# Optimization experiments

Hardware: AMD Instinct MI355X
Metric: run time of the kernel (lower is better)

## Reference

```python
import jax, jax.numpy as jnp
import numpy as np

H = 64   # hidden size
V = 29   # vocab / feature size
SOS = 27 # start-token index set to 1 in the initial one-hot


def _cell(x, h, c, Wih, Whh, bih, bhh):
    # PyTorch LSTMCell gate order: i, f, g, o
    g = x @ Wih.T + h @ Whh.T + bih + bhh
    i, f, gg, o = jnp.split(g, 4, axis=-1)
    c = jax.nn.sigmoid(f) * c + jax.nn.sigmoid(i) * jnp.tanh(gg)
    h = jax.nn.sigmoid(o) * jnp.tanh(c)
    return h, c


def setup_inputs() -> dict:
    key = jax.random.key(0)
    ks = iter(jax.random.split(key, 32))
    T, B = 1024, 512
    def p(shape, scale=0.05):
        return jax.random.normal(next(ks), shape, dtype=jnp.float32) * scale
    inp = {"input_seq": jax.random.normal(next(ks), (T, B, V), dtype=jnp.float32)}
    inp.update(
        enc_Wih0=p((4 * H, V)), enc_Whh0=p((4 * H, H)), enc_bih0=p((4 * H,)), enc_bhh0=p((4 * H,)),
        enc_Wih1=p((4 * H, H)), enc_Whh1=p((4 * H, H)), enc_bih1=p((4 * H,)), enc_bhh1=p((4 * H,)),
        d1_Wih=p((4 * H, V)), d1_Whh=p((4 * H, H)), d1_bih=p((4 * H,)), d1_bhh=p((4 * H,)),
        d2_Wih=p((4 * H, H)), d2_Whh=p((4 * H, H)), d2_bih=p((4 * H,)), d2_bhh=p((4 * H,)),
        cls_W=p((V, H)), cls_b=p((V,)),
    )
    return inp


def reference(input_seq, enc_Wih0, enc_Whh0, enc_bih0, enc_bhh0,
              enc_Wih1, enc_Whh1, enc_bih1, enc_bhh1,
              d1_Wih, d1_Whh, d1_bih, d1_bhh,
              d2_Wih, d2_Whh, d2_bih, d2_bhh,
              cls_W, cls_b):
    T, B, _ = input_seq.shape
    dt = input_seq.dtype
    z = jnp.zeros((B, H), dt)

    def layer(x_seq, Wih, Whh, bih, bhh):
        def step(carry, x):
            h, c = _cell(x, carry[0], carry[1], Wih, Whh, bih, bhh)
            return (h, c), h
        (h, c), ys = jax.lax.scan(step, (z, z), x_seq)
        return ys, h, c

    # 2-layer encoder LSTM with zero initial state
    y1, _, _ = layer(input_seq, enc_Wih0, enc_Whh0, enc_bih0, enc_bhh0)
    _, h1, c1 = layer(y1, enc_Wih1, enc_Whh1, enc_bih1, enc_bhh1)  # top-layer final (h, c)

    let0 = jnp.zeros((B, V), dt).at[:, SOS].set(1.0)

    def dec_step(carry, _):
        h1, c1, h2, c2, let = carry
        h1, c1 = _cell(let, h1, c1, d1_Wih, d1_Whh, d1_bih, d1_bhh)
        h2, c2 = _cell(h1, h2, c2, d2_Wih, d2_Whh, d2_bih, d2_bhh)
        pred = h2 @ cls_W.T + cls_b  # [B, V]
        idx = jnp.argmax(pred, axis=-1)  # [B]
        # Faithful to original bug: sets column idx[b] to 1 for ALL rows, for each b
        let = jnp.zeros((B, V), pred.dtype).at[:, idx].set(1.0)
        return (h1, c1, h2, c2, let), pred

    _, outputs = jax.lax.scan(dec_step, (h1, c1, z, z, let0), None, length=T)
    return outputs  # [T, B, V]
```

## Files before the change

### kernel.cpp

```cpp
#include <hip/hip_runtime.h>
#include <math.h>

#define TSTEPS 1024
#define BATCH  512
#define HID    64
#define VOC    29
#define SOS    27
#define MASK29 0x1FFFFFFFu

#define ENC_BLOCKS 256
#define DEC_BLOCKS 256
#define NTHREADS   512

__device__ __forceinline__ float frcp(float x){ return __builtin_amdgcn_rcpf(x); }
__device__ __forceinline__ float sigmf(float x){ return frcp(1.0f + __expf(-x)); }
__device__ __forceinline__ float tanhfast(float x){ return 1.0f - 2.0f*frcp(1.0f + __expf(2.0f*x)); }

__global__ __attribute__((amdgpu_flat_work_group_size(NTHREADS,NTHREADS), amdgpu_waves_per_eu(2,2)))
void enc_kernel(const float* __restrict__ x,
                const float* __restrict__ Wih0, const float* __restrict__ Whh0,
                const float* __restrict__ bih0, const float* __restrict__ bhh0,
                const float* __restrict__ Wih1, const float* __restrict__ Whh1,
                const float* __restrict__ bih1, const float* __restrict__ bhh1,
                float* __restrict__ h1g, float* __restrict__ c1g)
{
  const int tid = threadIdx.x;
  const int b0  = blockIdx.x * 2;
  const bool g0 = tid < 256;
  const int  r  = g0 ? tid : (tid-256);

  __shared__ __align__(16) float xs[2][32];
  __shared__ __align__(16) float h0s[2][HID], h1s[2][HID];
  __shared__ __align__(16) float gA[2][256], gB[2][256];

  float wh[64], w2[64];
  if (g0){
    #pragma unroll
    for (int k=0;k<64;k++) wh[k] = Whh0[r*64+k];
    #pragma unroll
    for (int k=0;k<29;k++) w2[k] = Wih0[r*29+k];
    #pragma unroll
    for (int k=29;k<64;k++) w2[k] = 0.f;
  } else {
    #pragma unroll
    for (int k=0;k<64;k++){ wh[k] = Whh1[r*64+k]; w2[k] = Wih1[r*64+k]; }
  }
  const float bias = g0 ? (bih0[r]+bhh0[r]) : (bih1[r]+bhh1[r]);

  float creg = 0.f;
  if (tid < 128){ int u=tid>>6,k=tid&63; h0s[u][k]=0.f; h1s[u][k]=0.f; }

  const int pidx = tid - 448;
  const bool pf  = (pidx >= 0) && (pidx < 2*VOC);
  const int prow = pf ? (pidx/VOC) : 0;
  const int pcol = pf ? (pidx%VOC) : 0;
  if (pf) xs[prow][pcol] = x[(size_t)(b0+prow)*VOC + pcol];
  __syncthreads();

  for (int t=0;t<=TSTEPS;t++){
    float xv = 0.f;
    if (pf && t+1 < TSTEPS)
      xv = x[(size_t)(t+1)*BATCH*VOC + (size_t)(b0+prow)*VOC + pcol];

    if (g0){
      if (t < TSTEPS){
        #pragma unroll
        for (int u=0;u<2;u++){
          float a0=bias,a1=0.f,a2=0.f,a3=0.f;
          const float4* xv4 = (const float4*)xs[u];
          #pragma unroll
          for (int c=0;c<7;c++){
            float4 q=xv4[c];
            a0=fmaf(q.x,w2[4*c+0],a0); a1=fmaf(q.y,w2[4*c+1],a1);
            a2=fmaf(q.z,w2[4*c+2],a2); a3=fmaf(q.w,w2[4*c+3],a3);
          }
          a0=fmaf(xs[u][28],w2[28],a0);
          const float4* h4=(const float4*)h0s[u];
          #pragma unroll
          for (int c=0;c<16;c++){
            float4 q=h4[c];
            a0=fmaf(q.x,wh[4*c+0],a0); a1=fmaf(q.y,wh[4*c+1],a1);
            a2=fmaf(q.z,wh[4*c+2],a2); a3=fmaf(q.w,wh[4*c+3],a3);
          }
          gA[u][r]=(a0+a1)+(a2+a3);
        }
      }
    } else {
      if (t >= 1){
        #pragma unroll
        for (int u=0;u<2;u++){
          float a0=bias,a1=0.f,a2=0.f,a3=0.f;
          const float4* i4=(const float4*)h0s[u];
          const float4* h4=(const float4*)h1s[u];
          #pragma unroll
          for (int c=0;c<16;c++){
            float4 q=i4[c], w=h4[c];
            a0=fmaf(q.x,w2[4*c+0],a0); a1=fmaf(q.y,w2[4*c+1],a1);
            a2=fmaf(q.z,w2[4*c+2],a2); a3=fmaf(q.w,w2[4*c+3],a3);
            a0=fmaf(w.x,wh[4*c+0],a0); a1=fmaf(w.y,wh[4*c+1],a1);
            a2=fmaf(w.z,wh[4*c+2],a2); a3=fmaf(w.w,wh[4*c+3],a3);
          }
          gB[u][r]=(a0+a1)+(a2+a3);
        }
      }
    }
    __syncthreads();
    if (tid < 128){
      if (t < TSTEPS){
        int u=tid>>6,k=tid&63;
        float ig=gA[u][k],fg=gA[u][64+k],gg=gA[u][128+k],og=gA[u][192+k];
        float c=sigmf(fg)*creg + sigmf(ig)*tanhfast(gg);
        creg=c; h0s[u][k]=sigmf(og)*tanhfast(c);
      }
    } else if (tid < 384){
      if (t >= 1){
        int tt=tid-256,u=tt>>6,k=tt&63;
        float ig=gB[u][k],fg=gB[u][64+k],gg=gB[u][128+k],og=gB[u][192+k];
        float c=sigmf(fg)*creg + sigmf(ig)*tanhfast(gg);
        creg=c; h1s[u][k]=sigmf(og)*tanhfast(c);
      }
    }
    if (pf && t+1 < TSTEPS) xs[prow][pcol] = xv;
    __syncthreads();
  }

  if (tid >= 256 && tid < 384){
    int tt=tid-256,u=tt>>6,k=tt&63;
    h1g[(b0+u)*HID+k]=h1s[u][k];
    c1g[(b0+u)*HID+k]=creg;
  }
}

__global__ __attribute__((amdgpu_flat_work_group_size(NTHREADS,NTHREADS), amdgpu_waves_per_eu(2,2)))
void dec_kernel(const float* __restrict__ h1gp, const float* __restrict__ c1gp,
                const float* __restrict__ W1ih, const float* __restrict__ W1hh,
                const float* __restrict__ b1ih, const float* __restrict__ b1hh,
                const float* __restrict__ W2ih, const float* __restrict__ W2hh,
                const float* __restrict__ b2ih, const float* __restrict__ b2hh,
                const float* __restrict__ clsW, const float* __restrict__ clsb,
                float* __restrict__ out,
                unsigned long long* __restrict__ lvl1)
{
  const int tid  = threadIdx.x;
  const int r    = tid >> 1;
  const int p    = tid & 1;
  const int b0   = blockIdx.x * 2;
  const unsigned grp = blockIdx.x & 15;
  const unsigned idx = blockIdx.x >> 4;

  __shared__ __align__(16) float clsW_s[VOC][68];
  __shared__ __align__(16) float clsb_s[32];
  __shared__ __align__(16) float gl[2][256];
  __shared__ __align__(16) float h1s[2][HID], h2s[2][HID];
  __shared__ unsigned maskLDS;

  for (int i=tid;i<VOC*HID;i+=NTHREADS) clsW_s[i/HID][i%HID] = clsW[i];
  if (tid<VOC) clsb_s[tid]=clsb[tid];

  float w1h[32], w2i[32], w2h[32], wi1c[15];
  #pragma unroll
  for (int k=0;k<32;k++){
    w1h[k]=W1hh[r*HID+32*p+k];
    w2i[k]=W2ih[r*HID+32*p+k];
    w2h[k]=W2hh[r*HID+32*p+k];
  }
  const int cbase = p ? 15 : 0;
  const int cn    = p ? 14 : 15;
  #pragma unroll
  for (int j=0;j<15;j++) wi1c[j] = (j<cn) ? W1ih[r*VOC+cbase+j] : 0.f;
  const float biasg = p ? 0.f : (b1ih[r]+b1hh[r]);
  const float bias2 = p ? 0.f : (b2ih[r]+b2hh[r]);

  float c1reg=0.f, c2reg=0.f;
  if (tid<128){
    int u=tid>>6,k=tid&63;
    h1s[u][k]=h1gp[(b0+u)*HID+k];
    c1reg    =c1gp[(b0+u)*HID+k];
    h2s[u][k]=0.f;
  }
  __syncthreads();

  float hd1[2];
  #pragma unroll
  for (int u=0;u<2;u++){
    float a0=0.f,a1=0.f,a2=0.f,a3=0.f;
    const float4* h4=(const float4*)(h1s[u]+32*p);
    #pragma unroll
    for (int c=0;c<8;c++){
      float4 q=h4[c];
      a0=fmaf(q.x,w1h[4*c+0],a0); a1=fmaf(q.y,w1h[4*c+1],a1);
      a2=fmaf(q.z,w1h[4*c+2],a2); a3=fmaf(q.w,w1h[4*c+3],a3);
    }
    hd1[u]=(a0+a1)+(a2+a3);
  }

  unsigned mask = 1u<<SOS;

  for (int s=0;s<TSTEPS;s++){
    #pragma unroll
    for (int u=0;u<2;u++){
      float it = biasg;
      #pragma unroll
      for (int j=0;j<15;j++)
        it += ((mask>>(cbase+j))&1u) ? wi1c[j] : 0.f;
      float v = it + hd1[u];
      v += __shfl_xor(v,1);
      if (!p) gl[u][r] = v;
    }
    __syncthreads();
    if (tid<128){
      int u=tid>>6,k=tid&63;
      float ig=gl[u][k],fg=gl[u][64+k],gg=gl[u][128+k],og=gl[u][192+k];
      float c=sigmf(fg)*c1reg+sigmf(ig)*tanhfast(gg);
      c1reg=c; h1s[u][k]=sigmf(og)*tanhfast(c);
    }
    __syncthreads();
    #pragma unroll
    for (int u=0;u<2;u++){
      float a0=bias2,a1=0.f,a2=0.f,a3=0.f;
      const float4* i4=(const float4*)(h1s[u]+32*p);
      const float4* h4=(const float4*)(h2s[u]+32*p);
      #pragma unroll
      for (int c=0;c<8;c++){
        float4 q=i4[c], w=h4[c];
        a0=fmaf(q.x,w2i[4*c+0],a0); a1=fmaf(q.y,w2i[4*c+1],a1);
        a2=fmaf(q.z,w2i[4*c+2],a2); a3=fmaf(q.w,w2i[4*c+3],a3);
        a0=fmaf(w.x,w2h[4*c+0],a0); a1=fmaf(w.y,w2h[4*c+1],a1);
        a2=fmaf(w.z,w2h[4*c+2],a2); a3=fmaf(w.w,w2h[4*c+3],a3);
      }
      float v=(a0+a1)+(a2+a3);
      v += __shfl_xor(v,1);
      if (!p) gl[u][r]=v;
    }
    __syncthreads();
    if (tid<128){
      int u=tid>>6,k=tid&63;
      float ig=gl[u][k],fg=gl[u][64+k],gg=gl[u][128+k],og=gl[u][192+k];
      float c=sigmf(fg)*c2reg+sigmf(ig)*tanhfast(gg);
      c2reg=c; h2s[u][k]=sigmf(og)*tanhfast(c);
    }
    __syncthreads();
    if (tid<64){
      int row=tid>>5, v=tid&31;
      float pv = -INFINITY;
      if (v<VOC){
        float a0=clsb_s[v],a1=0.f,a2=0.f,a3=0.f;
        const float4* h4=(const float4*)h2s[row];
        #pragma unroll
        for (int c=0;c<16;c++){
          float4 q=h4[c];
          a0=fmaf(q.x,clsW_s[v][4*c+0],a0); a1=fmaf(q.y,clsW_s[v][4*c+1],a1);
          a2=fmaf(q.z,clsW_s[v][4*c+2],a2); a3=fmaf(q.w,clsW_s[v][4*c+3],a3);
        }
        pv=(a0+a1)+(a2+a3);
        out[((size_t)s*BATCH + (size_t)(b0+row))*VOC + v]=pv;
      }
      int ix=v;
      #pragma unroll
      for (int off=16; off>0; off>>=1){
        float ov=__shfl_xor(pv,off);
        int   oi=__shfl_xor(ix,off);
        if (ov>pv || (ov==pv && oi<ix)){ pv=ov; ix=oi; }
      }
      unsigned bit = 1u<<ix;
      unsigned mb  = bit | __shfl_xor(bit,32);
      if (tid==0 && s+1<TSTEPS)
        __hip_atomic_fetch_or(&lvl1[(size_t)grp*TSTEPS+s],
                              (unsigned long long)mb | (1ULL<<(32+idx)),
                              __ATOMIC_RELAXED, __HIP_MEMORY_SCOPE_AGENT);
    }
    if (s+1<TSTEPS){
      #pragma unroll
      for (int u=0;u<2;u++){
        float a0=0.f,a1=0.f,a2=0.f,a3=0.f;
        const float4* h4=(const float4*)(h1s[u]+32*p);
        #pragma unroll
        for (int c=0;c<8;c++){
          float4 q=h4[c];
          a0=fmaf(q.x,w1h[4*c+0],a0); a1=fmaf(q.y,w1h[4*c+1],a1);
          a2=fmaf(q.z,w1h[4*c+2],a2); a3=fmaf(q.w,w1h[4*c+3],a3);
        }
        hd1[u]=(a0+a1)+(a2+a3);
      }
      if (tid<64){
        while (true){
          unsigned long long u64 = 0;
          if (tid<16)
            u64 = __hip_atomic_load(&lvl1[(size_t)tid*TSTEPS+s],
                                    __ATOMIC_RELAXED, __HIP_MEMORY_SCOPE_AGENT);
          bool ok = (tid>=16) || ((unsigned)(u64>>32) == 0xFFFFu);
          if (__ballot(ok) == ~0ull){
            unsigned m = (tid<16) ? ((unsigned)u64 & MASK29) : 0u;
            m |= __shfl_xor(m,1); m |= __shfl_xor(m,2);
            m |= __shfl_xor(m,4); m |= __shfl_xor(m,8);
            if (tid==0) maskLDS = m;
            break;
          }
        }
      }
      __syncthreads();
      mask = maskLDS;
    }
  }
}

extern "C" void kernel_launch(void* const* d_in, const int* in_sizes, int n_in,
                              void* d_out, int out_size, void* d_ws, size_t ws_size,
                              hipStream_t stream)
{
  const float* x     = (const float*)d_in[0];
  const float* eWih0 = (const float*)d_in[1];
  const float* eWhh0 = (const float*)d_in[2];
  const float* ebih0 = (const float*)d_in[3];
  const float* ebhh0 = (const float*)d_in[4];
  const float* eWih1 = (const float*)d_in[5];
  const float* eWhh1 = (const float*)d_in[6];
  const float* ebih1 = (const float*)d_in[7];
  const float* ebhh1 = (const float*)d_in[8];
  const float* d1Wih = (const float*)d_in[9];
  const float* d1Whh = (const float*)d_in[10];
  const float* d1bih = (const float*)d_in[11];
  const float* d1bhh = (const float*)d_in[12];
  const float* d2Wih = (const float*)d_in[13];
  const float* d2Whh = (const float*)d_in[14];
  const float* d2bih = (const float*)d_in[15];
  const float* d2bhh = (const float*)d_in[16];
  const float* clsW  = (const float*)d_in[17];
  const float* clsb  = (const float*)d_in[18];
  float* out = (float*)d_out;

  float* h1g = (float*)d_ws;
  float* c1g = h1g + BATCH*HID;
  unsigned long long* lvl1 = (unsigned long long*)((char*)d_ws + (size_t)(2*BATCH*HID)*sizeof(float));

  hipMemsetAsync(lvl1, 0, 16*TSTEPS*sizeof(unsigned long long), stream);

  enc_kernel<<<ENC_BLOCKS, NTHREADS, 0, stream>>>(
      x, eWih0,eWhh0,ebih0,ebhh0, eWih1,eWhh1,ebih1,ebhh1, h1g,c1g);

  void* args[] = { (void*)&h1g, (void*)&c1g,
                   (void*)&d1Wih,(void*)&d1Whh,(void*)&d1bih,(void*)&d1bhh,
                   (void*)&d2Wih,(void*)&d2Whh,(void*)&d2bih,(void*)&d2bhh,
                   (void*)&clsW,(void*)&clsb,(void*)&out,(void*)&lvl1 };
  hipLaunchCooperativeKernel((void*)dec_kernel, dim3(DEC_BLOCKS), dim3(NTHREADS),
                             args, 0, stream);
}
```

Measured before the change: 5.881 ms.

## Restructure encoder to one batch row per block and fuse decoder gate activations

The encoder now gives each block a single batch row: two threads per gate row split the dot product, and layer 0 and layer 1 run one after the other within a timestep. It launches 512 blocks with waves_per_eu raised to 4. The decoder now assigns four threads per hidden unit, each holding all four gates. After a shuffle reduction every thread applies the activations itself, which removes the separate gate-to-LDS exchange and two barriers per step. The input-weight table moves to LDS and h2 is double-buffered. The encoder now has a longer serial chain per step (two sequential layers with four barriers), and the decoder uses more registers and LDS.

```diff
diff --git a/kernel.cpp b/kernel.cpp
--- a/kernel.cpp
+++ b/kernel.cpp
@@ -8,7 +8,7 @@
 #define SOS    27
 #define MASK29 0x1FFFFFFFu
 
-#define ENC_BLOCKS 256
+#define ENC_BLOCKS 512
 #define DEC_BLOCKS 256
 #define NTHREADS   512
 
@@ -16,7 +16,7 @@
 __device__ __forceinline__ float sigmf(float x){ return frcp(1.0f + __expf(-x)); }
 __device__ __forceinline__ float tanhfast(float x){ return 1.0f - 2.0f*frcp(1.0f + __expf(2.0f*x)); }
 
-__global__ __attribute__((amdgpu_flat_work_group_size(NTHREADS,NTHREADS), amdgpu_waves_per_eu(2,2)))
+__global__ __attribute__((amdgpu_flat_work_group_size(NTHREADS,NTHREADS), amdgpu_waves_per_eu(4,4)))
 void enc_kernel(const float* __restrict__ x,
                 const float* __restrict__ Wih0, const float* __restrict__ Whh0,
                 const float* __restrict__ bih0, const float* __restrict__ bhh0,
@@ -25,109 +25,99 @@
                 float* __restrict__ h1g, float* __restrict__ c1g)
 {
   const int tid = threadIdx.x;
-  const int b0  = blockIdx.x * 2;
-  const bool g0 = tid < 256;
-  const int  r  = g0 ? tid : (tid-256);
-
-  __shared__ __align__(16) float xs[2][32];
-  __shared__ __align__(16) float h0s[2][HID], h1s[2][HID];
-  __shared__ __align__(16) float gA[2][256], gB[2][256];
-
-  float wh[64], w2[64];
-  if (g0){
-    #pragma unroll
-    for (int k=0;k<64;k++) wh[k] = Whh0[r*64+k];
-    #pragma unroll
-    for (int k=0;k<29;k++) w2[k] = Wih0[r*29+k];
-    #pragma unroll
-    for (int k=29;k<64;k++) w2[k] = 0.f;
-  } else {
-    #pragma unroll
-    for (int k=0;k<64;k++){ wh[k] = Whh1[r*64+k]; w2[k] = Wih1[r*64+k]; }
-  }
-  const float bias = g0 ? (bih0[r]+bhh0[r]) : (bih1[r]+bhh1[r]);
+  const int r   = tid >> 1;
+  const int p   = tid & 1;
+  const int b0  = blockIdx.x;
+
+  __shared__ __align__(16) float xs[32];
+  __shared__ __align__(16) float g0[256];
+  __shared__ __align__(16) float h0s[HID], h1s[HID];
+
+  float w0h[32], w1i[32], w1h[32], w0i[15];
+  #pragma unroll
+  for (int k=0;k<32;k++){
+    w0h[k]=Whh0[r*HID+32*p+k];
+    w1i[k]=Wih1[r*HID+32*p+k];
+    w1h[k]=Whh1[r*HID+32*p+k];
+  }
+  const int cb = p*15, cn = p?14:15;
+  #pragma unroll
+  for (int j=0;j<15;j++) w0i[j] = (j<cn)? Wih0[r*VOC+cb+j] : 0.f;
+  const float bias0 = p?0.f:(bih0[r]+bhh0[r]);
+  const float bias1 = p?0.f:(bih1[r]+bhh1[r]);
 
   float creg = 0.f;
-  if (tid < 128){ int u=tid>>6,k=tid&63; h0s[u][k]=0.f; h1s[u][k]=0.f; }
-
-  const int pidx = tid - 448;
-  const bool pf  = (pidx >= 0) && (pidx < 2*VOC);
-  const int prow = pf ? (pidx/VOC) : 0;
-  const int pcol = pf ? (pidx%VOC) : 0;
-  if (pf) xs[prow][pcol] = x[(size_t)(b0+prow)*VOC + pcol];
+  if (tid<64) h0s[tid]=0.f;
+  if (tid>=64 && tid<128) h1s[tid-64]=0.f;
+  if (tid>=186 && tid<189) xs[29+(tid-186)]=0.f;
+
+  const int pfc = tid-128;
+  const bool ispf = (pfc>=0) && (pfc<VOC);
+  if (ispf) xs[pfc] = x[(size_t)b0*VOC + pfc];
   __syncthreads();
 
-  for (int t=0;t<=TSTEPS;t++){
-    float xv = 0.f;
-    if (pf && t+1 < TSTEPS)
-      xv = x[(size_t)(t+1)*BATCH*VOC + (size_t)(b0+prow)*VOC + pcol];
-
-    if (g0){
-      if (t < TSTEPS){
-        #pragma unroll
-        for (int u=0;u<2;u++){
-          float a0=bias,a1=0.f,a2=0.f,a3=0.f;
-          const float4* xv4 = (const float4*)xs[u];
-          #pragma unroll
-          for (int c=0;c<7;c++){
-            float4 q=xv4[c];
-            a0=fmaf(q.x,w2[4*c+0],a0); a1=fmaf(q.y,w2[4*c+1],a1);
-            a2=fmaf(q.z,w2[4*c+2],a2); a3=fmaf(q.w,w2[4*c+3],a3);
-          }
-          a0=fmaf(xs[u][28],w2[28],a0);
-          const float4* h4=(const float4*)h0s[u];
-          #pragma unroll
-          for (int c=0;c<16;c++){
-            float4 q=h4[c];
-            a0=fmaf(q.x,wh[4*c+0],a0); a1=fmaf(q.y,wh[4*c+1],a1);
-            a2=fmaf(q.z,wh[4*c+2],a2); a3=fmaf(q.w,wh[4*c+3],a3);
-          }
-          gA[u][r]=(a0+a1)+(a2+a3);
-        }
-      }
-    } else {
-      if (t >= 1){
-        #pragma unroll
-        for (int u=0;u<2;u++){
-          float a0=bias,a1=0.f,a2=0.f,a3=0.f;
-          const float4* i4=(const float4*)h0s[u];
-          const float4* h4=(const float4*)h1s[u];
-          #pragma unroll
-          for (int c=0;c<16;c++){
-            float4 q=i4[c], w=h4[c];
-            a0=fmaf(q.x,w2[4*c+0],a0); a1=fmaf(q.y,w2[4*c+1],a1);
-            a2=fmaf(q.z,w2[4*c+2],a2); a3=fmaf(q.w,w2[4*c+3],a3);
-            a0=fmaf(w.x,wh[4*c+0],a0); a1=fmaf(w.y,wh[4*c+1],a1);
-            a2=fmaf(w.z,wh[4*c+2],a2); a3=fmaf(w.w,wh[4*c+3],a3);
-          }
-          gB[u][r]=(a0+a1)+(a2+a3);
-        }
-      }
-    }
-    __syncthreads();
-    if (tid < 128){
-      if (t < TSTEPS){
-        int u=tid>>6,k=tid&63;
-        float ig=gA[u][k],fg=gA[u][64+k],gg=gA[u][128+k],og=gA[u][192+k];
-        float c=sigmf(fg)*creg + sigmf(ig)*tanhfast(gg);
-        creg=c; h0s[u][k]=sigmf(og)*tanhfast(c);
-      }
-    } else if (tid < 384){
-      if (t >= 1){
-        int tt=tid-256,u=tt>>6,k=tt&63;
-        float ig=gB[u][k],fg=gB[u][64+k],gg=gB[u][128+k],og=gB[u][192+k];
-        float c=sigmf(fg)*creg + sigmf(ig)*tanhfast(gg);
-        creg=c; h1s[u][k]=sigmf(og)*tanhfast(c);
-      }
-    }
-    if (pf && t+1 < TSTEPS) xs[prow][pcol] = xv;
-    __syncthreads();
-  }
-
-  if (tid >= 256 && tid < 384){
-    int tt=tid-256,u=tt>>6,k=tt&63;
-    h1g[(b0+u)*HID+k]=h1s[u][k];
-    c1g[(b0+u)*HID+k]=creg;
+  for (int t=0;t<TSTEPS;t++){
+    float xn=0.f;
+    if (ispf && t+1<TSTEPS)
+      xn = x[(size_t)(t+1)*BATCH*VOC + (size_t)b0*VOC + pfc];
+
+    {
+      float a0=bias0,a1=0.f,a2=0.f,a3=0.f;
+      #pragma unroll
+      for (int j=0;j<15;j++){
+        float acc = fmaf(xs[cb+j], w0i[j], (j&3)==0?a0:((j&3)==1?a1:((j&3)==2?a2:a3)));
+        if ((j&3)==0) a0=acc; else if ((j&3)==1) a1=acc; else if ((j&3)==2) a2=acc; else a3=acc;
+      }
+      const float4* hv=(const float4*)(h0s+32*p);
+      #pragma unroll
+      for (int c=0;c<8;c++){
+        float4 q=hv[c];
+        a0=fmaf(q.x,w0h[4*c+0],a0); a1=fmaf(q.y,w0h[4*c+1],a1);
+        a2=fmaf(q.z,w0h[4*c+2],a2); a3=fmaf(q.w,w0h[4*c+3],a3);
+      }
+      float v=(a0+a1)+(a2+a3);
+      v += __shfl_xor(v,1);
+      if (!p) g0[r]=v;
+    }
+    __syncthreads();
+    if (tid<64){
+      int k=tid;
+      float ig=g0[k],fg=g0[64+k],gg=g0[128+k],og=g0[192+k];
+      float c=sigmf(fg)*creg+sigmf(ig)*tanhfast(gg);
+      creg=c; h0s[k]=sigmf(og)*tanhfast(c);
+    }
+    __syncthreads();
+    {
+      float a0=bias1,a1=0.f,a2=0.f,a3=0.f;
+      const float4* iv=(const float4*)(h0s+32*p);
+      const float4* hv=(const float4*)(h1s+32*p);
+      #pragma unroll
+      for (int c=0;c<8;c++){
+        float4 q=iv[c], w=hv[c];
+        a0=fmaf(q.x,w1i[4*c+0],a0); a1=fmaf(q.y,w1i[4*c+1],a1);
+        a2=fmaf(q.z,w1i[4*c+2],a2); a3=fmaf(q.w,w1i[4*c+3],a3);
+        a0=fmaf(w.x,w1h[4*c+0],a0); a1=fmaf(w.y,w1h[4*c+1],a1);
+        a2=fmaf(w.z,w1h[4*c+2],a2); a3=fmaf(w.w,w1h[4*c+3],a3);
+      }
+      float v=(a0+a1)+(a2+a3);
+      v += __shfl_xor(v,1);
+      if (!p) g0[r]=v;
+    }
+    __syncthreads();
+    if (tid>=64 && tid<128){
+      int k=tid-64;
+      float ig=g0[k],fg=g0[64+k],gg=g0[128+k],og=g0[192+k];
+      float c=sigmf(fg)*creg+sigmf(ig)*tanhfast(gg);
+      creg=c; h1s[k]=sigmf(og)*tanhfast(c);
+    }
+    if (ispf && t+1<TSTEPS) xs[pfc]=xn;
+    __syncthreads();
+  }
+
+  if (tid>=64 && tid<128){
+    int k=tid-64;
+    h1g[b0*HID+k]=h1s[k];
+    c1g[b0*HID+k]=creg;
   }
 }
 
@@ -141,116 +131,140 @@
                 float* __restrict__ out,
                 unsigned long long* __restrict__ lvl1)
 {
-  const int tid  = threadIdx.x;
-  const int r    = tid >> 1;
-  const int p    = tid & 1;
-  const int b0   = blockIdx.x * 2;
+  const int tid = threadIdx.x;
+  const int u   = tid >> 8;
+  const int j   = (tid >> 2) & 63;
+  const int q   = tid & 3;
+  const int b0  = blockIdx.x * 2;
   const unsigned grp = blockIdx.x & 15;
   const unsigned idx = blockIdx.x >> 4;
 
   __shared__ __align__(16) float clsW_s[VOC][68];
   __shared__ __align__(16) float clsb_s[32];
-  __shared__ __align__(16) float gl[2][256];
-  __shared__ __align__(16) float h1s[2][HID], h2s[2][HID];
+  __shared__ __align__(16) float w1iq[4*8*256];
+  __shared__ __align__(16) float h1s[2][HID];
+  __shared__ __align__(16) float h2s[2][2][HID];
   __shared__ unsigned maskLDS;
 
-  for (int i=tid;i<VOC*HID;i+=NTHREADS) clsW_s[i/HID][i%HID] = clsW[i];
+  for (int i=tid;i<VOC*HID;i+=NTHREADS) clsW_s[i/HID][i%HID]=clsW[i];
   if (tid<VOC) clsb_s[tid]=clsb[tid];
-
-  float w1h[32], w2i[32], w2h[32], wi1c[15];
+  for (int i=tid;i<4*8*256;i+=NTHREADS){
+    int gg=i>>11, cc=(i>>8)&7, l=i&255, jj=l>>2, qq=l&3;
+    int col=qq*8+cc;
+    w1iq[i] = (col<VOC)? W1ih[(gg*64+jj)*VOC+col] : 0.f;
+  }
+
+  float w1h[64], w2i[64], w2h[64];
   #pragma unroll
-  for (int k=0;k<32;k++){
-    w1h[k]=W1hh[r*HID+32*p+k];
-    w2i[k]=W2ih[r*HID+32*p+k];
-    w2h[k]=W2hh[r*HID+32*p+k];
-  }
-  const int cbase = p ? 15 : 0;
-  const int cn    = p ? 14 : 15;
+  for (int g=0;g<4;g++){
+    const int row=g*64+j, cidx=q*16;
+    #pragma unroll
+    for (int c=0;c<16;c++){
+      w1h[g*16+c]=W1hh[row*HID+cidx+c];
+      w2i[g*16+c]=W2ih[row*HID+cidx+c];
+      w2h[g*16+c]=W2hh[row*HID+cidx+c];
+    }
+  }
+  float bs1[4], bs2[4];
   #pragma unroll
-  for (int j=0;j<15;j++) wi1c[j] = (j<cn) ? W1ih[r*VOC+cbase+j] : 0.f;
-  const float biasg = p ? 0.f : (b1ih[r]+b1hh[r]);
-  const float bias2 = p ? 0.f : (b2ih[r]+b2hh[r]);
-
-  float c1reg=0.f, c2reg=0.f;
+  for (int g=0;g<4;g++){
+    bs1[g]=b1ih[g*64+j]+b1hh[g*64+j];
+    bs2[g]=b2ih[g*64+j]+b2hh[g*64+j];
+  }
+
+  float c1 = c1gp[(b0+u)*HID+j];
+  float c2 = 0.f;
   if (tid<128){
-    int u=tid>>6,k=tid&63;
-    h1s[u][k]=h1gp[(b0+u)*HID+k];
-    c1reg    =c1gp[(b0+u)*HID+k];
-    h2s[u][k]=0.f;
+    int uu=tid>>6,k=tid&63;
+    h1s[uu][k]=h1gp[(b0+uu)*HID+k];
+    h2s[0][uu][k]=0.f;
   }
   __syncthreads();
 
-  float hd1[2];
-  #pragma unroll
-  for (int u=0;u<2;u++){
-    float a0=0.f,a1=0.f,a2=0.f,a3=0.f;
-    const float4* h4=(const float4*)(h1s[u]+32*p);
+  float hd1[4];
+  {
+    const float4* H=(const float4*)&h1s[u][q*16];
+    float4 H0=H[0],H1=H[1],H2=H[2],H3=H[3];
     #pragma unroll
-    for (int c=0;c<8;c++){
-      float4 q=h4[c];
-      a0=fmaf(q.x,w1h[4*c+0],a0); a1=fmaf(q.y,w1h[4*c+1],a1);
-      a2=fmaf(q.z,w1h[4*c+2],a2); a3=fmaf(q.w,w1h[4*c+3],a3);
-    }
-    hd1[u]=(a0+a1)+(a2+a3);
+    for (int g=0;g<4;g++){
+      const float* w=&w1h[g*16];
+      float a=0.f;
+      a=fmaf(H0.x,w[0],a); a=fmaf(H0.y,w[1],a); a=fmaf(H0.z,w[2],a); a=fmaf(H0.w,w[3],a);
+      a=fmaf(H1.x,w[4],a); a=fmaf(H1.y,w[5],a); a=fmaf(H1.z,w[6],a); a=fmaf(H1.w,w[7],a);
+      a=fmaf(H2.x,w[8],a); a=fmaf(H2.y,w[9],a); a=fmaf(H2.z,w[10],a); a=fmaf(H2.w,w[11],a);
+      a=fmaf(H3.x,w[12],a); a=fmaf(H3.y,w[13],a); a=fmaf(H3.z,w[14],a); a=fmaf(H3.w,w[15],a);
+      hd1[g]=a;
+    }
   }
 
   unsigned mask = 1u<<SOS;
 
   for (int s=0;s<TSTEPS;s++){
-    #pragma unroll
-    for (int u=0;u<2;u++){
-      float it = biasg;
-      #pragma unroll
-      for (int j=0;j<15;j++)
-        it += ((mask>>(cbase+j))&1u) ? wi1c[j] : 0.f;
-      float v = it + hd1[u];
-      v += __shfl_xor(v,1);
-      if (!p) gl[u][r] = v;
-    }
-    __syncthreads();
-    if (tid<128){
-      int u=tid>>6,k=tid&63;
-      float ig=gl[u][k],fg=gl[u][64+k],gg=gl[u][128+k],og=gl[u][192+k];
-      float c=sigmf(fg)*c1reg+sigmf(ig)*tanhfast(gg);
-      c1reg=c; h1s[u][k]=sigmf(og)*tanhfast(c);
-    }
-    __syncthreads();
-    #pragma unroll
-    for (int u=0;u<2;u++){
-      float a0=bias2,a1=0.f,a2=0.f,a3=0.f;
-      const float4* i4=(const float4*)(h1s[u]+32*p);
-      const float4* h4=(const float4*)(h2s[u]+32*p);
-      #pragma unroll
-      for (int c=0;c<8;c++){
-        float4 q=i4[c], w=h4[c];
-        a0=fmaf(q.x,w2i[4*c+0],a0); a1=fmaf(q.y,w2i[4*c+1],a1);
-        a2=fmaf(q.z,w2i[4*c+2],a2); a3=fmaf(q.w,w2i[4*c+3],a3);
-        a0=fmaf(w.x,w2h[4*c+0],a0); a1=fmaf(w.y,w2h[4*c+1],a1);
-        a2=fmaf(w.z,w2h[4*c+2],a2); a3=fmaf(w.w,w2h[4*c+3],a3);
-      }
-      float v=(a0+a1)+(a2+a3);
-      v += __shfl_xor(v,1);
-      if (!p) gl[u][r]=v;
-    }
-    __syncthreads();
-    if (tid<128){
-      int u=tid>>6,k=tid&63;
-      float ig=gl[u][k],fg=gl[u][64+k],gg=gl[u][128+k],og=gl[u][192+k];
-      float c=sigmf(fg)*c2reg+sigmf(ig)*tanhfast(gg);
-      c2reg=c; h2s[u][k]=sigmf(og)*tanhfast(c);
-    }
-    __syncthreads();
+    const int rb = s&1, wb = rb^1;
+
+    {
+      const unsigned mq = (mask>>(q*8)) & 0xFFu;
+      float gv[4];
+      #pragma unroll
+      for (int g=0;g<4;g++){
+        float a = hd1[g] + (q==0 ? bs1[g] : 0.f);
+        #pragma unroll
+        for (int cc=0;cc<8;cc++){
+          float w = w1iq[((g*8+cc)<<8) + (tid&255)];
+          a += ((mq>>cc)&1u) ? w : 0.f;
+        }
+        gv[g]=a;
+      }
+      #pragma unroll
+      for (int g=0;g<4;g++){ gv[g]+=__shfl_xor(gv[g],1); gv[g]+=__shfl_xor(gv[g],2); }
+      float ig=sigmf(gv[0]), fg=sigmf(gv[1]), gg=tanhfast(gv[2]), og=sigmf(gv[3]);
+      c1 = fg*c1 + ig*gg;
+      float h = og*tanhfast(c1);
+      if (q==0) h1s[u][j]=h;
+    }
+    __syncthreads();
+
+    {
+      const float4* A=(const float4*)&h1s[u][q*16];
+      const float4* B=(const float4*)&h2s[rb][u][q*16];
+      float4 A0=A[0],A1=A[1],A2=A[2],A3=A[3];
+      float4 B0=B[0],B1=B[1],B2=B[2],B3=B[3];
+      float gv[4];
+      #pragma unroll
+      for (int g=0;g<4;g++){
+        const float* wi=&w2i[g*16];
+        const float* wh=&w2h[g*16];
+        float a = (q==0 ? bs2[g] : 0.f);
+        a=fmaf(A0.x,wi[0],a); a=fmaf(A0.y,wi[1],a); a=fmaf(A0.z,wi[2],a); a=fmaf(A0.w,wi[3],a);
+        a=fmaf(A1.x,wi[4],a); a=fmaf(A1.y,wi[5],a); a=fmaf(A1.z,wi[6],a); a=fmaf(A1.w,wi[7],a);
+        a=fmaf(A2.x,wi[8],a); a=fmaf(A2.y,wi[9],a); a=fmaf(A2.z,wi[10],a); a=fmaf(A2.w,wi[11],a);
+        a=fmaf(A3.x,wi[12],a); a=fmaf(A3.y,wi[13],a); a=fmaf(A3.z,wi[14],a); a=fmaf(A3.w,wi[15],a);
+        a=fmaf(B0.x,wh[0],a); a=fmaf(B0.y,wh[1],a); a=fmaf(B0.z,wh[2],a); a=fmaf(B0.w,wh[3],a);
+        a=fmaf(B1.x,wh[4],a); a=fmaf(B1.y,wh[5],a); a=fmaf(B1.z,wh[6],a); a=fmaf(B1.w,wh[7],a);
+        a=fmaf(B2.x,wh[8],a); a=fmaf(B2.y,wh[9],a); a=fmaf(B2.z,wh[10],a); a=fmaf(B2.w,wh[11],a);
+        a=fmaf(B3.x,wh[12],a); a=fmaf(B3.y,wh[13],a); a=fmaf(B3.z,wh[14],a); a=fmaf(B3.w,wh[15],a);
+        gv[g]=a;
+      }
+      #pragma unroll
+      for (int g=0;g<4;g++){ gv[g]+=__shfl_xor(gv[g],1); gv[g]+=__shfl_xor(gv[g],2); }
+      float ig=sigmf(gv[0]), fg=sigmf(gv[1]), gg=tanhfast(gv[2]), og=sigmf(gv[3]);
+      c2 = fg*c2 + ig*gg;
+      float h = og*tanhfast(c2);
+      if (q==0) h2s[wb][u][j]=h;
+    }
+    __syncthreads();
+
     if (tid<64){
       int row=tid>>5, v=tid&31;
-      float pv = -INFINITY;
+      float pv=-INFINITY;
       if (v<VOC){
         float a0=clsb_s[v],a1=0.f,a2=0.f,a3=0.f;
-        const float4* h4=(const float4*)h2s[row];
+        const float4* h4=(const float4*)h2s[wb][row];
         #pragma unroll
         for (int c=0;c<16;c++){
-          float4 q=h4[c];
-          a0=fmaf(q.x,clsW_s[v][4*c+0],a0); a1=fmaf(q.y,clsW_s[v][4*c+1],a1);
-          a2=fmaf(q.z,clsW_s[v][4*c+2],a2); a3=fmaf(q.w,clsW_s[v][4*c+3],a3);
+          float4 qq=h4[c];
+          a0=fmaf(qq.x,clsW_s[v][4*c+0],a0); a1=fmaf(qq.y,clsW_s[v][4*c+1],a1);
+          a2=fmaf(qq.z,clsW_s[v][4*c+2],a2); a3=fmaf(qq.w,clsW_s[v][4*c+3],a3);
         }
         pv=(a0+a1)+(a2+a3);
         out[((size_t)s*BATCH + (size_t)(b0+row))*VOC + v]=pv;
@@ -269,19 +283,21 @@
                               (unsigned long long)mb | (1ULL<<(32+idx)),
                               __ATOMIC_RELAXED, __HIP_MEMORY_SCOPE_AGENT);
     }
+    {
+      const float4* H=(const float4*)&h1s[u][q*16];
+      float4 H0=H[0],H1=H[1],H2=H[2],H3=H[3];
+      #pragma unroll
+      for (int g=0;g<4;g++){
+        const float* w=&w1h[g*16];
+        float a=0.f;
+        a=fmaf(H0.x,w[0],a); a=fmaf(H0.y,w[1],a); a=fmaf(H0.z,w[2],a); a=fmaf(H0.w,w[3],a);
+        a=fmaf(H1.x,w[4],a); a=fmaf(H1.y,w[5],a); a=fmaf(H1.z,w[6],a); a=fmaf(H1.w,w[7],a);
+        a=fmaf(H2.x,w[8],a); a=fmaf(H2.y,w[9],a); a=fmaf(H2.z,w[10],a); a=fmaf(H2.w,w[11],a);
+        a=fmaf(H3.x,w[12],a); a=fmaf(H3.y,w[13],a); a=fmaf(H3.z,w[14],a); a=fmaf(H3.w,w[15],a);
+        hd1[g]=a;
+      }
+    }
     if (s+1<TSTEPS){
-      #pragma unroll
-      for (int u=0;u<2;u++){
-        float a0=0.f,a1=0.f,a2=0.f,a3=0.f;
-        const float4* h4=(const float4*)(h1s[u]+32*p);
-        #pragma unroll
-        for (int c=0;c<8;c++){
-          float4 q=h4[c];
-          a0=fmaf(q.x,w1h[4*c+0],a0); a1=fmaf(q.y,w1h[4*c+1],a1);
-          a2=fmaf(q.z,w1h[4*c+2],a2); a3=fmaf(q.w,w1h[4*c+3],a3);
-        }
-        hd1[u]=(a0+a1)+(a2+a3);
-      }
       if (tid<64){
         while (true){
           unsigned long long u64 = 0;
```

New measurement: 12.09 ms. +105.7%, slower.

## Fuse gate activations via lane shuffles and replace decoder barrier with LDS flag

Applied to the files above, without the earlier changes.

Both kernels remap threads so eight lanes cover the four gates of one hidden unit. Gate values are exchanged with xor shuffles, so every thread applies the LSTM nonlinearity itself and the separate shared-memory gate buffers and their barriers go away. Double-buffered hidden-state arrays remove the extra barrier per step, which lets the encoder run both layers in one step instead of skewing them. In the decoder, the inter-block mask exchange moves to 32 groups of 8 blocks, and the post-wait __syncthreads is replaced by an LDS tag-flag spin with s_sleep. The trade-off is redundant activation math on every lane, plus spin-polling risk and more subtle memory-ordering assumptions.

```diff
diff --git a/kernel.cpp b/kernel.cpp
--- a/kernel.cpp
+++ b/kernel.cpp
@@ -15,6 +15,20 @@
 __device__ __forceinline__ float frcp(float x){ return __builtin_amdgcn_rcpf(x); }
 __device__ __forceinline__ float sigmf(float x){ return frcp(1.0f + __expf(-x)); }
 __device__ __forceinline__ float tanhfast(float x){ return 1.0f - 2.0f*frcp(1.0f + __expf(2.0f*x)); }
+
+__device__ __forceinline__ void gate_gather(float v, int g, float&i, float&f, float&gg, float&o){
+  float b = __shfl_xor(v,2);
+  float c = __shfl_xor(v,4);
+  float d = __shfl_xor(v,6);
+  i  = (g==0)?v:(g==1)?b:(g==2)?c:d;
+  f  = (g==1)?v:(g==0)?b:(g==3)?c:d;
+  gg = (g==2)?v:(g==3)?b:(g==0)?c:d;
+  o  = (g==3)?v:(g==2)?b:(g==1)?c:d;
+}
+__device__ __forceinline__ float lstm_act(float i,float f,float g,float o,float&c){
+  c = sigmf(f)*c + sigmf(i)*tanhfast(g);
+  return sigmf(o)*tanhfast(c);
+}
 
 __global__ __attribute__((amdgpu_flat_work_group_size(NTHREADS,NTHREADS), amdgpu_waves_per_eu(2,2)))
 void enc_kernel(const float* __restrict__ x,
@@ -25,109 +39,98 @@
                 float* __restrict__ h1g, float* __restrict__ c1g)
 {
   const int tid = threadIdx.x;
+  const int k   = tid >> 3;
+  const int l   = tid & 7;
+  const int g   = l >> 1;
+  const int p   = l & 1;
   const int b0  = blockIdx.x * 2;
-  const bool g0 = tid < 256;
-  const int  r  = g0 ? tid : (tid-256);
+  const int row = g*64 + k;
 
   __shared__ __align__(16) float xs[2][32];
-  __shared__ __align__(16) float h0s[2][HID], h1s[2][HID];
-  __shared__ __align__(16) float gA[2][256], gB[2][256];
-
-  float wh[64], w2[64];
-  if (g0){
-    #pragma unroll
-    for (int k=0;k<64;k++) wh[k] = Whh0[r*64+k];
-    #pragma unroll
-    for (int k=0;k<29;k++) w2[k] = Wih0[r*29+k];
-    #pragma unroll
-    for (int k=29;k<64;k++) w2[k] = 0.f;
-  } else {
-    #pragma unroll
-    for (int k=0;k<64;k++){ wh[k] = Whh1[r*64+k]; w2[k] = Wih1[r*64+k]; }
-  }
-  const float bias = g0 ? (bih0[r]+bhh0[r]) : (bih1[r]+bhh1[r]);
-
-  float creg = 0.f;
-  if (tid < 128){ int u=tid>>6,k=tid&63; h0s[u][k]=0.f; h1s[u][k]=0.f; }
-
-  const int pidx = tid - 448;
-  const bool pf  = (pidx >= 0) && (pidx < 2*VOC);
-  const int prow = pf ? (pidx/VOC) : 0;
-  const int pcol = pf ? (pidx%VOC) : 0;
-  if (pf) xs[prow][pcol] = x[(size_t)(b0+prow)*VOC + pcol];
+  __shared__ __align__(16) float h0s[2][2][HID], h1s[2][2][HID];
+
+  float w0i[15], w0h[32], w1i[32], w1h[32];
+  #pragma unroll
+  for (int j=0;j<15;j++) w0i[j] = (p && j==14) ? 0.f : Wih0[row*VOC + p*15 + j];
+  #pragma unroll
+  for (int j=0;j<32;j++){
+    w0h[j]=Whh0[row*HID+32*p+j];
+    w1i[j]=Wih1[row*HID+32*p+j];
+    w1h[j]=Whh1[row*HID+32*p+j];
+  }
+  const float bias0 = p?0.f:(bih0[row]+bhh0[row]);
+  const float bias1 = p?0.f:(bih1[row]+bhh1[row]);
+
+  float c0[2]={0.f,0.f}, c1[2]={0.f,0.f}, hlast[2]={0.f,0.f};
+  if (tid<128){ int uu=tid>>6,kk=tid&63; h0s[1][uu][kk]=0.f; h1s[1][uu][kk]=0.f; }
+  if (tid>=128 && tid<134){ int z=tid-128; xs[z>=3][29+(z%3)]=0.f; }
+
+  const bool ispf = tid < 2*VOC;
+  const int  xb   = (tid >= VOC) ? 1 : 0;
+  const int  xk   = tid - xb*VOC;
+  if (ispf) xs[xb][xk] = x[(size_t)(b0+xb)*VOC + xk];
   __syncthreads();
 
-  for (int t=0;t<=TSTEPS;t++){
-    float xv = 0.f;
-    if (pf && t+1 < TSTEPS)
-      xv = x[(size_t)(t+1)*BATCH*VOC + (size_t)(b0+prow)*VOC + pcol];
-
-    if (g0){
-      if (t < TSTEPS){
-        #pragma unroll
-        for (int u=0;u<2;u++){
-          float a0=bias,a1=0.f,a2=0.f,a3=0.f;
-          const float4* xv4 = (const float4*)xs[u];
-          #pragma unroll
-          for (int c=0;c<7;c++){
-            float4 q=xv4[c];
-            a0=fmaf(q.x,w2[4*c+0],a0); a1=fmaf(q.y,w2[4*c+1],a1);
-            a2=fmaf(q.z,w2[4*c+2],a2); a3=fmaf(q.w,w2[4*c+3],a3);
-          }
-          a0=fmaf(xs[u][28],w2[28],a0);
-          const float4* h4=(const float4*)h0s[u];
-          #pragma unroll
-          for (int c=0;c<16;c++){
-            float4 q=h4[c];
-            a0=fmaf(q.x,wh[4*c+0],a0); a1=fmaf(q.y,wh[4*c+1],a1);
-            a2=fmaf(q.z,wh[4*c+2],a2); a3=fmaf(q.w,wh[4*c+3],a3);
-          }
-          gA[u][r]=(a0+a1)+(a2+a3);
-        }
-      }
-    } else {
-      if (t >= 1){
-        #pragma unroll
-        for (int u=0;u<2;u++){
-          float a0=bias,a1=0.f,a2=0.f,a3=0.f;
-          const float4* i4=(const float4*)h0s[u];
-          const float4* h4=(const float4*)h1s[u];
-          #pragma unroll
-          for (int c=0;c<16;c++){
-            float4 q=i4[c], w=h4[c];
-            a0=fmaf(q.x,w2[4*c+0],a0); a1=fmaf(q.y,w2[4*c+1],a1);
-            a2=fmaf(q.z,w2[4*c+2],a2); a3=fmaf(q.w,w2[4*c+3],a3);
-            a0=fmaf(w.x,wh[4*c+0],a0); a1=fmaf(w.y,wh[4*c+1],a1);
-            a2=fmaf(w.z,wh[4*c+2],a2); a3=fmaf(w.w,wh[4*c+3],a3);
-          }
-          gB[u][r]=(a0+a1)+(a2+a3);
-        }
-      }
+  for (int t=0;t<TSTEPS;t++){
+    const int rb=(t&1)^1, wb=t&1;
+    float xn=0.f;
+    if (ispf && t+1<TSTEPS)
+      xn = x[(size_t)(t+1)*BATCH*VOC + (size_t)(b0+xb)*VOC + xk];
+
+    #pragma unroll
+    for (int u=0;u<2;u++){
+      float a0=bias0,a1=0.f,a2=0.f,a3=0.f;
+      #pragma unroll
+      for (int j=0;j<15;j++){
+        float t0 = xs[u][p*15+j]*w0i[j];
+        if ((j&3)==0) a0+=t0; else if ((j&3)==1) a1+=t0; else if ((j&3)==2) a2+=t0; else a3+=t0;
+      }
+      const float4* hv=(const float4*)&h0s[rb][u][32*p];
+      #pragma unroll
+      for (int c=0;c<8;c++){
+        float4 q=hv[c];
+        a0=fmaf(q.x,w0h[4*c+0],a0); a1=fmaf(q.y,w0h[4*c+1],a1);
+        a2=fmaf(q.z,w0h[4*c+2],a2); a3=fmaf(q.w,w0h[4*c+3],a3);
+      }
+      float v=(a0+a1)+(a2+a3);
+      v += __shfl_xor(v,1);
+      float ig,fg,gg,og;
+      gate_gather(v,g,ig,fg,gg,og);
+      float h = lstm_act(ig,fg,gg,og,c0[u]);
+      if (l==0) h0s[wb][u][k]=h;
     }
     __syncthreads();
-    if (tid < 128){
-      if (t < TSTEPS){
-        int u=tid>>6,k=tid&63;
-        float ig=gA[u][k],fg=gA[u][64+k],gg=gA[u][128+k],og=gA[u][192+k];
-        float c=sigmf(fg)*creg + sigmf(ig)*tanhfast(gg);
-        creg=c; h0s[u][k]=sigmf(og)*tanhfast(c);
-      }
-    } else if (tid < 384){
-      if (t >= 1){
-        int tt=tid-256,u=tt>>6,k=tt&63;
-        float ig=gB[u][k],fg=gB[u][64+k],gg=gB[u][128+k],og=gB[u][192+k];
-        float c=sigmf(fg)*creg + sigmf(ig)*tanhfast(gg);
-        creg=c; h1s[u][k]=sigmf(og)*tanhfast(c);
-      }
-    }
-    if (pf && t+1 < TSTEPS) xs[prow][pcol] = xv;
+    #pragma unroll
+    for (int u=0;u<2;u++){
+      float a0=bias1,a1=0.f,a2=0.f,a3=0.f;
+      const float4* iv=(const float4*)&h0s[wb][u][32*p];
+      const float4* hv=(const float4*)&h1s[rb][u][32*p];
+      #pragma unroll
+      for (int c=0;c<8;c++){
+        float4 q=iv[c], w=hv[c];
+        a0=fmaf(q.x,w1i[4*c+0],a0); a1=fmaf(q.y,w1i[4*c+1],a1);
+        a2=fmaf(q.z,w1i[4*c+2],a2); a3=fmaf(q.w,w1i[4*c+3],a3);
+        a0=fmaf(w.x,w1h[4*c+0],a0); a1=fmaf(w.y,w1h[4*c+1],a1);
+        a2=fmaf(w.z,w1h[4*c+2],a2); a3=fmaf(w.w,w1h[4*c+3],a3);
+      }
+      float v=(a0+a1)+(a2+a3);
+      v += __shfl_xor(v,1);
+      float ig,fg,gg,og;
+      gate_gather(v,g,ig,fg,gg,og);
+      float h = lstm_act(ig,fg,gg,og,c1[u]);
+      hlast[u]=h;
+      if (l==0) h1s[wb][u][k]=h;
+    }
+    if (ispf && t+1<TSTEPS) xs[xb][xk]=xn;
     __syncthreads();
   }
 
-  if (tid >= 256 && tid < 384){
-    int tt=tid-256,u=tt>>6,k=tt&63;
-    h1g[(b0+u)*HID+k]=h1s[u][k];
-    c1g[(b0+u)*HID+k]=creg;
+  if (l==0){
+    #pragma unroll
+    for (int u=0;u<2;u++){
+      h1g[(b0+u)*HID+k]=hlast[u];
+      c1g[(b0+u)*HID+k]=c1[u];
+    }
   }
 }
 
@@ -141,42 +144,44 @@
                 float* __restrict__ out,
                 unsigned long long* __restrict__ lvl1)
 {
-  const int tid  = threadIdx.x;
-  const int r    = tid >> 1;
-  const int p    = tid & 1;
-  const int b0   = blockIdx.x * 2;
-  const unsigned grp = blockIdx.x & 15;
-  const unsigned idx = blockIdx.x >> 4;
+  const int tid = threadIdx.x;
+  const int k   = tid >> 3;
+  const int l   = tid & 7;
+  const int g   = l >> 1;
+  const int p   = l & 1;
+  const int b0  = blockIdx.x * 2;
+  const unsigned grp = blockIdx.x & 31;
+  const unsigned idx = blockIdx.x >> 5;
+  const int row = g*64 + k;
 
   __shared__ __align__(16) float clsW_s[VOC][68];
   __shared__ __align__(16) float clsb_s[32];
-  __shared__ __align__(16) float gl[2][256];
-  __shared__ __align__(16) float h1s[2][HID], h2s[2][HID];
-  __shared__ unsigned maskLDS;
-
-  for (int i=tid;i<VOC*HID;i+=NTHREADS) clsW_s[i/HID][i%HID] = clsW[i];
+  __shared__ __align__(16) float h1s[2][2][HID], h2s[2][2][HID];
+  __shared__ unsigned mask2;
+
+  for (int i=tid;i<VOC*HID;i+=NTHREADS) clsW_s[i/HID][i%HID]=clsW[i];
   if (tid<VOC) clsb_s[tid]=clsb[tid];
-
-  float w1h[32], w2i[32], w2h[32], wi1c[15];
-  #pragma unroll
-  for (int k=0;k<32;k++){
-    w1h[k]=W1hh[r*HID+32*p+k];
-    w2i[k]=W2ih[r*HID+32*p+k];
-    w2h[k]=W2hh[r*HID+32*p+k];
-  }
-  const int cbase = p ? 15 : 0;
-  const int cn    = p ? 14 : 15;
-  #pragma unroll
-  for (int j=0;j<15;j++) wi1c[j] = (j<cn) ? W1ih[r*VOC+cbase+j] : 0.f;
-  const float biasg = p ? 0.f : (b1ih[r]+b1hh[r]);
-  const float bias2 = p ? 0.f : (b2ih[r]+b2hh[r]);
-
-  float c1reg=0.f, c2reg=0.f;
+  if (tid==0) __hip_atomic_store(&mask2, 0u, __ATOMIC_RELAXED, __HIP_MEMORY_SCOPE_WORKGROUP);
+
+  float wi1c[15], w1h[32], w2i[32], w2h[32];
+  #pragma unroll
+  for (int j=0;j<15;j++) wi1c[j] = (p && j==14) ? 0.f : W1ih[row*VOC + p*15 + j];
+  #pragma unroll
+  for (int j=0;j<32;j++){
+    w1h[j]=W1hh[row*HID+32*p+j];
+    w2i[j]=W2ih[row*HID+32*p+j];
+    w2h[j]=W2hh[row*HID+32*p+j];
+  }
+  const float bs1 = p?0.f:(b1ih[row]+b1hh[row]);
+  const float bs2 = p?0.f:(b2ih[row]+b2hh[row]);
+
+  float c1[2], c2[2]={0.f,0.f};
+  #pragma unroll
+  for (int u=0;u<2;u++) c1[u] = c1gp[(b0+u)*HID+k];
   if (tid<128){
-    int u=tid>>6,k=tid&63;
-    h1s[u][k]=h1gp[(b0+u)*HID+k];
-    c1reg    =c1gp[(b0+u)*HID+k];
-    h2s[u][k]=0.f;
+    int uu=tid>>6,kk=tid&63;
+    h1s[1][uu][kk]=h1gp[(b0+uu)*HID+kk];
+    h2s[1][uu][kk]=0.f;
   }
   __syncthreads();
 
@@ -184,10 +189,10 @@
   #pragma unroll
   for (int u=0;u<2;u++){
     float a0=0.f,a1=0.f,a2=0.f,a3=0.f;
-    const float4* h4=(const float4*)(h1s[u]+32*p);
+    const float4* hv=(const float4*)&h1s[1][u][32*p];
     #pragma unroll
     for (int c=0;c<8;c++){
-      float4 q=h4[c];
+      float4 q=hv[c];
       a0=fmaf(q.x,w1h[4*c+0],a0); a1=fmaf(q.y,w1h[4*c+1],a1);
       a2=fmaf(q.z,w1h[4*c+2],a2); a3=fmaf(q.w,w1h[4*c+3],a3);
     }
@@ -197,32 +202,30 @@
   unsigned mask = 1u<<SOS;
 
   for (int s=0;s<TSTEPS;s++){
-    #pragma unroll
-    for (int u=0;u<2;u++){
-      float it = biasg;
+    const int wb=s&1, rb2=wb^1;
+
+    #pragma unroll
+    for (int u=0;u<2;u++){
+      float v = hd1[u] + bs1;
       #pragma unroll
       for (int j=0;j<15;j++)
-        it += ((mask>>(cbase+j))&1u) ? wi1c[j] : 0.f;
-      float v = it + hd1[u];
+        v += ((mask>>(p*15+j))&1u) ? wi1c[j] : 0.f;
       v += __shfl_xor(v,1);
-      if (!p) gl[u][r] = v;
+      float ig,fg,gg,og;
+      gate_gather(v,g,ig,fg,gg,og);
+      float h = lstm_act(ig,fg,gg,og,c1[u]);
+      if (l==0) h1s[wb][u][k]=h;
     }
     __syncthreads();
-    if (tid<128){
-      int u=tid>>6,k=tid&63;
-      float ig=gl[u][k],fg=gl[u][64+k],gg=gl[u][128+k],og=gl[u][192+k];
-      float c=sigmf(fg)*c1reg+sigmf(ig)*tanhfast(gg);
-      c1reg=c; h1s[u][k]=sigmf(og)*tanhfast(c);
-    }
-    __syncthreads();
-    #pragma unroll
-    for (int u=0;u<2;u++){
-      float a0=bias2,a1=0.f,a2=0.f,a3=0.f;
-      const float4* i4=(const float4*)(h1s[u]+32*p);
-      const float4* h4=(const float4*)(h2s[u]+32*p);
+
+    #pragma unroll
+    for (int u=0;u<2;u++){
+      float a0=bs2,a1=0.f,a2=0.f,a3=0.f;
+      const float4* iv=(const float4*)&h1s[wb][u][32*p];
+      const float4* hv=(const float4*)&h2s[rb2][u][32*p];
       #pragma unroll
       for (int c=0;c<8;c++){
-        float4 q=i4[c], w=h4[c];
+        float4 q=iv[c], w=hv[c];
         a0=fmaf(q.x,w2i[4*c+0],a0); a1=fmaf(q.y,w2i[4*c+1],a1);
         a2=fmaf(q.z,w2i[4*c+2],a2); a3=fmaf(q.w,w2i[4*c+3],a3);
         a0=fmaf(w.x,w2h[4*c+0],a0); a1=fmaf(w.y,w2h[4*c+1],a1);
@@ -230,32 +233,29 @@
       }
       float v=(a0+a1)+(a2+a3);
       v += __shfl_xor(v,1);
-      if (!p) gl[u][r]=v;
+      float ig,fg,gg,og;
+      gate_gather(v,g,ig,fg,gg,og);
+      float h = lstm_act(ig,fg,gg,og,c2[u]);
+      if (l==0) h2s[wb][u][k]=h;
     }
     __syncthreads();
-    if (tid<128){
-      int u=tid>>6,k=tid&63;
-      float ig=gl[u][k],fg=gl[u][64+k],gg=gl[u][128+k],og=gl[u][192+k];
-      float c=sigmf(fg)*c2reg+sigmf(ig)*tanhfast(gg);
-      c2reg=c; h2s[u][k]=sigmf(og)*tanhfast(c);
-    }
-    __syncthreads();
+
     if (tid<64){
-      int row=tid>>5, v=tid&31;
-      float pv = -INFINITY;
-      if (v<VOC){
-        float a0=clsb_s[v],a1=0.f,a2=0.f,a3=0.f;
-        const float4* h4=(const float4*)h2s[row];
+      int row2=tid>>5, v2=tid&31;
+      float pv=-INFINITY;
+      if (v2<VOC){
+        float a0=clsb_s[v2],a1=0.f,a2=0.f,a3=0.f;
+        const float4* h4=(const float4*)h2s[wb][row2];
         #pragma unroll
         for (int c=0;c<16;c++){
           float4 q=h4[c];
-          a0=fmaf(q.x,clsW_s[v][4*c+0],a0); a1=fmaf(q.y,clsW_s[v][4*c+1],a1);
-          a2=fmaf(q.z,clsW_s[v][4*c+2],a2); a3=fmaf(q.w,clsW_s[v][4*c+3],a3);
+          a0=fmaf(q.x,clsW_s[v2][4*c+0],a0); a1=fmaf(q.y,clsW_s[v2][4*c+1],a1);
+          a2=fmaf(q.z,clsW_s[v2][4*c+2],a2); a3=fmaf(q.w,clsW_s[v2][4*c+3],a3);
         }
         pv=(a0+a1)+(a2+a3);
-        out[((size_t)s*BATCH + (size_t)(b0+row))*VOC + v]=pv;
-      }
-      int ix=v;
+        out[((size_t)s*BATCH + (size_t)(b0+row2))*VOC + v2]=pv;
+      }
+      int ix=v2;
       #pragma unroll
       for (int off=16; off>0; off>>=1){
         float ov=__shfl_xor(pv,off);
@@ -269,37 +269,48 @@
                               (unsigned long long)mb | (1ULL<<(32+idx)),
                               __ATOMIC_RELAXED, __HIP_MEMORY_SCOPE_AGENT);
     }
+    #pragma unroll
+    for (int u=0;u<2;u++){
+      float a0=0.f,a1=0.f,a2=0.f,a3=0.f;
+      const float4* hv=(const float4*)&h1s[wb][u][32*p];
+      #pragma unroll
+      for (int c=0;c<8;c++){
+        float4 q=hv[c];
+        a0=fmaf(q.x,w1h[4*c+0],a0); a1=fmaf(q.y,w1h[4*c+1],a1);
+        a2=fmaf(q.z,w1h[4*c+2],a2); a3=fmaf(q.w,w1h[4*c+3],a3);
+      }
+      hd1[u]=(a0+a1)+(a2+a3);
+    }
     if (s+1<TSTEPS){
-      #pragma unroll
-      for (int u=0;u<2;u++){
-        float a0=0.f,a1=0.f,a2=0.f,a3=0.f;
-        const float4* h4=(const float4*)(h1s[u]+32*p);
-        #pragma unroll
-        for (int c=0;c<8;c++){
-          float4 q=h4[c];
-          a0=fmaf(q.x,w1h[4*c+0],a0); a1=fmaf(q.y,w1h[4*c+1],a1);
-          a2=fmaf(q.z,w1h[4*c+2],a2); a3=fmaf(q.w,w1h[4*c+3],a3);
-        }
-        hd1[u]=(a0+a1)+(a2+a3);
-      }
+      const unsigned tag = (unsigned)((s&1)+1);
       if (tid<64){
+        unsigned m;
         while (true){
-          unsigned long long u64 = 0;
-          if (tid<16)
-            u64 = __hip_atomic_load(&lvl1[(size_t)tid*TSTEPS+s],
-                                    __ATOMIC_RELAXED, __HIP_MEMORY_SCOPE_AGENT);
-          bool ok = (tid>=16) || ((unsigned)(u64>>32) == 0xFFFFu);
+          unsigned long long u64 =
+            __hip_atomic_load(&lvl1[(size_t)(tid&31)*TSTEPS+s],
+                              __ATOMIC_RELAXED, __HIP_MEMORY_SCOPE_AGENT);
+          bool ok = ((unsigned)(u64>>32) == 0xFFu);
           if (__ballot(ok) == ~0ull){
-            unsigned m = (tid<16) ? ((unsigned)u64 & MASK29) : 0u;
-            m |= __shfl_xor(m,1); m |= __shfl_xor(m,2);
-            m |= __shfl_xor(m,4); m |= __shfl_xor(m,8);
-            if (tid==0) maskLDS = m;
+            m = (unsigned)u64 & MASK29;
+            m |= __shfl_xor(m,1);  m |= __shfl_xor(m,2);
+            m |= __shfl_xor(m,4);  m |= __shfl_xor(m,8);
+            m |= __shfl_xor(m,16);
             break;
           }
+          __builtin_amdgcn_s_sleep(1);
         }
-      }
-      __syncthreads();
-      mask = maskLDS;
+        mask = m;
+        if (tid==0)
+          __hip_atomic_store(&mask2, m | (tag<<29),
+                             __ATOMIC_RELAXED, __HIP_MEMORY_SCOPE_WORKGROUP);
+      } else {
+        unsigned val;
+        do {
+          __builtin_amdgcn_s_sleep(1);
+          val = __hip_atomic_load(&mask2, __ATOMIC_RELAXED, __HIP_MEMORY_SCOPE_WORKGROUP);
+        } while ((val>>29) != tag);
+        mask = val & MASK29;
+      }
     }
   }
 }
@@ -333,7 +344,7 @@
   float* c1g = h1g + BATCH*HID;
   unsigned long long* lvl1 = (unsigned long long*)((char*)d_ws + (size_t)(2*BATCH*HID)*sizeof(float));
 
-  hipMemsetAsync(lvl1, 0, 16*TSTEPS*sizeof(unsigned long long), stream);
+  hipMemsetAsync(lvl1, 0, 32*TSTEPS*sizeof(unsigned long long), stream);
 
   enc_kernel<<<ENC_BLOCKS, NTHREADS, 0, stream>>>(
       x, eWih0,eWhh0,ebih0,ebhh0, eWih1,eWhh1,ebih1,ebhh1, h1g,c1g);
```

New measurement: 7.510 ms. +27.7%, slower.
